# Performance work log

Measured on AMD Instinct MI355X. Metric: run time of the kernel, lower is better.

The kernel has to match this reference:

```python
import jax, jax.numpy as jnp
import numpy as np

N_WAY = 5
K_SHOT = 5
SEQ = 196          # patch tokens per image (ViT-S/16 @ 224)
TEMP = 0.0510310363  # similarity temperature ~ 1/sqrt(384)
LR = 0.1
OPT_STEPS = 15


def _normalize(emb):
    # [B, S, D] -> [B*S, D], rows L2-normalized with 1e-8 floor (matches torch.max(norm, 1e-8))
    v = emb.reshape(-1, emb.shape[-1])
    n = jnp.linalg.norm(v, axis=1, keepdims=True)
    return v / jnp.maximum(n, 1e-8)


def _block_mask():
    # block_diag of (SEQ x SEQ) blocks of -100 for each of the n_way*k_shot support images
    return jnp.kron(jnp.eye(N_WAY * K_SHOT, dtype=jnp.float32),
                    jnp.ones((SEQ, SEQ), jnp.float32)) * (-100.0)


def _predict(sup, qry, v, mask):
    # sup: [n_way*k_shot, S, D], qry: [Qb, Qs, D], v: [n_way*k_shot*S]
    S = sup.shape[1]
    Qb, Qs = qry.shape[0], qry.shape[1]
    C = _normalize(sup) @ _normalize(qry).T           # [Ls, Qb*Qs] cosine sims
    if mask is not None:
        C = C + mask
    pred = C + v[:, None]
    pred = pred.reshape(N_WAY, K_SHOT * S, Qb, Qs)
    pred = pred.transpose(0, 1, 3, 2).reshape(N_WAY, K_SHOT * S * Qs, Qb)
    pred = pred / TEMP
    pred = jax.scipy.special.logsumexp(pred, axis=1)  # [n_way, Qb]
    return pred.T                                     # [Qb, n_way]


def _optimize_v(sup_key, sup_query, labels, mask):
    # online SGD on the patch-embedding importance vector v (starts at zero)
    Ls = N_WAY * K_SHOT * sup_key.shape[1]
    B = sup_query.shape[0]

    def loss(v):
        p = _predict(sup_key, sup_query, v, mask)  # [B, n_way]
        logp = jax.nn.log_softmax(p, axis=1)
        return -jnp.mean(logp[jnp.arange(B), labels])

    def step(v, _):
        return v - LR * jax.grad(loss)(v), None

    v, _ = jax.lax.scan(step, jnp.zeros((Ls,), jnp.float32), None, length=OPT_STEPS)
    return v


def setup_inputs() -> dict:
    key = jax.random.key(0)
    k1, k2, k3, k4 = jax.random.split(key, 4)
    return {
        "support_emb_key": jax.random.normal(k1, (N_WAY * K_SHOT, SEQ, 384), jnp.float32),
        "support_emb_query": jax.random.normal(k2, (N_WAY * K_SHOT, SEQ, 384), jnp.float32),
        "query_emb": jax.random.normal(k3, (75, SEQ, 384), jnp.float32),
        "support_labels": jax.random.randint(k4, (N_WAY * K_SHOT,), 0, N_WAY, dtype=jnp.int32),
    }


def reference(support_emb_key, support_emb_query, query_emb, support_labels):
    mask = _block_mask()
    v = _optimize_v(support_emb_key, support_emb_query, support_labels, mask)
    return _predict(support_emb_key, query_emb, v, None)  # [75, n_way]
```

## Files before the change

kernel.cpp:

```cpp
#include <hip/hip_runtime.h>
#include <hip/hip_bf16.h>

#define NW 5
#define KS 5
#define SEQ 196
#define DIM 384
#define NSUP 25
#define NQRY 75
#define NIMG 100
#define LSUP 4900
#define LSUP_PAD 4992
#define QROWS 208
#define BLOCK_W 980
#define OPT_STEPS 15
#define MTILES 39
#define NSUPWG (NSUP * MTILES)
#define NQWG   (NQRY * MTILES)

static constexpr float TEMP_F = 0.0510310363f;
static constexpr float INV_T  = 1.0f / TEMP_F;
static constexpr float LR_F   = 0.1f;

typedef short v8s __attribute__((ext_vector_type(8)));
typedef float v4f __attribute__((ext_vector_type(4)));

__device__ inline unsigned short f2bf(float x) {
    unsigned int u = __float_as_uint(x);
    u += 0x7fffu + ((u >> 16) & 1u);
    return (unsigned short)(u >> 16);
}

__device__ __forceinline__ float fresh_f32(float* p) {
    return __hip_atomic_fetch_add(p, 0.0f, __ATOMIC_RELAXED, __HIP_MEMORY_SCOPE_AGENT);
}
__device__ __forceinline__ int fresh_i32(int* p) {
    return __hip_atomic_fetch_add(p, 0, __ATOMIC_RELAXED, __HIP_MEMORY_SCOPE_AGENT);
}
__device__ __forceinline__ unsigned fresh_u32(unsigned* p) {
    return __hip_atomic_fetch_add(p, 0u, __ATOMIC_RELAXED, __HIP_MEMORY_SCOPE_AGENT);
}

__global__ __launch_bounds__(256) void norm_all(const float* __restrict__ supk,
                                                const float* __restrict__ supq,
                                                const float* __restrict__ qry,
                                                unsigned short* __restrict__ Kb,
                                                unsigned short* __restrict__ Qall) {
    int R = blockIdx.x * 4 + (threadIdx.x >> 6);
    int l = threadIdx.x & 63;
    unsigned short* out;
    const float* in;
    float scale;
    if (R < LSUP_PAD) {
        out = Kb + (size_t)R * DIM;
        if (R >= LSUP) {
            #pragma unroll
            for (int k = 0; k < 6; ++k) out[l + 64 * k] = 0;
            return;
        }
        in = supk + (size_t)R * DIM;
        scale = INV_T;
    } else {
        int i = R - LSUP_PAD;
        int img = i / QROWS;
        int r = i - img * QROWS;
        out = Qall + (size_t)i * DIM;
        if (r >= SEQ) {
            #pragma unroll
            for (int k = 0; k < 6; ++k) out[l + 64 * k] = 0;
            return;
        }
        in = (img < NSUP)
            ? supq + ((size_t)img * SEQ + r) * DIM
            : qry  + ((size_t)(img - NSUP) * SEQ + r) * DIM;
        scale = 1.0f;
    }
    float x[6];
    #pragma unroll
    for (int k = 0; k < 6; ++k) x[k] = in[l + 64 * k];
    float s = 0.f;
    #pragma unroll
    for (int k = 0; k < 6; ++k) s += x[k] * x[k];
    #pragma unroll
    for (int m = 1; m < 64; m <<= 1) s += __shfl_xor(s, m);
    float sc = scale / fmaxf(sqrtf(s), 1e-8f);
    #pragma unroll
    for (int k = 0; k < 6; ++k) out[l + 64 * k] = f2bf(x[k] * sc);
}

#define MT  128
#define NTP 208
#define KCC 64

__device__ __forceinline__ void gload16(const void* g, void* l) {
    __builtin_amdgcn_global_load_lds(
        (__attribute__((address_space(1))) void*)g,
        (__attribute__((address_space(3))) void*)l, 16, 0, 0);
}

template<int IMG_BASE, int NWG, bool SUPPORT>
__device__ __forceinline__ void gemm_body(
    int gid,
    const unsigned short* __restrict__ Kb,
    const unsigned short* __restrict__ Qall,
    float* __restrict__ Rall,
    unsigned* done,
    unsigned short* Asm, unsigned short* Bsm)
{
    int t = threadIdx.x;

    constexpr int qq = NWG >> 3;
    constexpr int rr = NWG & 7;
    int xcd = gid & 7;
    int sub = gid >> 3;
    int L = (xcd < rr ? xcd * (qq + 1) : rr * (qq + 1) + (xcd - rr) * qq) + sub;
    int img = IMG_BASE + L / MTILES;
    int m_base = (L % MTILES) * MT;

    const unsigned short* Qimg = Qall + (size_t)img * (QROWS * DIM);

    int wv = t >> 6;
    int l  = t & 63;
    int lo = l & 15;
    int hi = l >> 4;
    int mh = (wv >> 1) * 64;
    int nh = wv & 1;

    int srow = l >> 3;
    int skp  = (l & 7) ^ srow;
    const unsigned short* aSrc = Kb   + (size_t)(m_base + wv * 32 + srow) * DIM + skp * 8;
    const unsigned short* bSrc = Qimg + (size_t)srow * DIM + skp * 8;

    v4f acc[4][7];
    #pragma unroll
    for (int m = 0; m < 4; ++m)
        #pragma unroll
        for (int n = 0; n < 7; ++n)
            acc[m][n] = (v4f){0.f, 0.f, 0.f, 0.f};

    for (int kb = 0; kb < DIM; kb += KCC) {
        #pragma unroll
        for (int j = 0; j < 4; ++j)
            gload16(aSrc + (size_t)j * 8 * DIM + kb,
                    Asm + (wv * 32 + j * 8) * KCC);
        #pragma unroll
        for (int jj = 0; jj < 7; ++jj) {
            int j = wv + jj * 4;
            if (j < 26)
                gload16(bSrc + (size_t)j * 8 * DIM + kb,
                        Bsm + j * 8 * KCC);
        }
        __syncthreads();

        const unsigned short* Ar = Asm + (mh + lo) * KCC;
        const unsigned short* Br = Bsm + (nh * 112 + lo) * KCC;
        #pragma unroll
        for (int kk = 0; kk < 2; ++kk) {
            int koff = ((hi + 4 * kk) ^ (lo & 7)) * 8;
            v8s a0 = *(const v8s*)(Ar + koff);
            v8s a1 = *(const v8s*)(Ar + 16 * KCC + koff);
            v8s a2 = *(const v8s*)(Ar + 32 * KCC + koff);
            v8s a3 = *(const v8s*)(Ar + 48 * KCC + koff);
            #pragma unroll
            for (int n = 0; n < 7; ++n) {
                if (nh == 0 || n < 6) {
                    v8s bb = *(const v8s*)(Br + n * 16 * KCC + koff);
                    acc[0][n] = __builtin_amdgcn_mfma_f32_16x16x32_bf16(a0, bb, acc[0][n], 0, 0, 0);
                    acc[1][n] = __builtin_amdgcn_mfma_f32_16x16x32_bf16(a1, bb, acc[1][n], 0, 0, 0);
                    acc[2][n] = __builtin_amdgcn_mfma_f32_16x16x32_bf16(a2, bb, acc[2][n], 0, 0, 0);
                    acc[3][n] = __builtin_amdgcn_mfma_f32_16x16x32_bf16(a3, bb, acc[3][n], 0, 0, 0);
                }
            }
        }
        __syncthreads();
    }

    float s[4][4];
    #pragma unroll
    for (int m = 0; m < 4; ++m)
        #pragma unroll
        for (int j = 0; j < 4; ++j) s[m][j] = 0.f;
    #pragma unroll
    for (int n = 0; n < 7; ++n) {
        if (nh == 0 || n < 6) {
            bool ok = ((nh * 7 + n) * 16 + lo) < SEQ;
            #pragma unroll
            for (int m = 0; m < 4; ++m)
                #pragma unroll
                for (int j = 0; j < 4; ++j)
                    s[m][j] += ok ? __expf(acc[m][n][j]) : 0.f;
        }
    }
    #pragma unroll
    for (int mm = 1; mm < 16; mm <<= 1) {
        #pragma unroll
        for (int m = 0; m < 4; ++m)
            #pragma unroll
            for (int j = 0; j < 4; ++j)
                s[m][j] += __shfl_xor(s[m][j], mm);
    }
    float* rp = (float*)Asm;
    if (lo == 0) {
        #pragma unroll
        for (int m = 0; m < 4; ++m)
            #pragma unroll
            for (int j = 0; j < 4; ++j)
                rp[nh * 128 + mh + m * 16 + hi * 4 + j] = s[m][j];
    }
    __syncthreads();
    if (t < MT) {
        int gr = m_base + t;
        if (gr < LSUP) {
            float o = rp[t] + rp[128 + t];
            if (img < NSUP && (gr / SEQ) == img) o = 0.f;
            if (SUPPORT)
                __hip_atomic_store(&Rall[(size_t)img * LSUP + gr], o,
                                   __ATOMIC_RELAXED, __HIP_MEMORY_SCOPE_AGENT);
            else
                Rall[(size_t)img * LSUP + gr] = o;
        }
    }
    if (SUPPORT) {
        __syncthreads();
        if (t == 0)
            __hip_atomic_fetch_add(done, 1u, __ATOMIC_RELAXED, __HIP_MEMORY_SCOPE_AGENT);
    }
}

__global__ __launch_bounds__(256, 3) void mega(
    const unsigned short* __restrict__ Kb,
    const unsigned short* __restrict__ Qall,
    float* __restrict__ Rall,
    const int* __restrict__ labels,
    float* __restrict__ Dbufs,
    int* __restrict__ flags,
    unsigned* __restrict__ done,
    float* __restrict__ e_out)
{
    __shared__ __align__(16) unsigned short Asm[MT * KCC];
    __shared__ __align__(16) unsigned short Bsm[NTP * KCC];

    if (blockIdx.x >= NW + NSUPWG) {
        gemm_body<NSUP, NQWG, false>((int)blockIdx.x - (NW + NSUPWG),
                                     Kb, Qall, Rall, done, Asm, Bsm);
        return;
    }
    if (blockIdx.x >= NW) {
        gemm_body<0, NSUPWG, true>((int)blockIdx.x - NW,
                                   Kb, Qall, Rall, done, Asm, Bsm);
        return;
    }

    float* sh  = (float*)Asm;
    float* red = sh;
    float* cfs = sh + 100;
    float* Dsm = sh + 128;
    int*   lsm = (int*)(sh + 256);

    int w = blockIdx.x;
    int t = threadIdx.x;
    int wave = t >> 6, lane = t & 63;

    if (t == 0) {
        while (fresh_u32(done) < (unsigned)NSUPWG)
            __builtin_amdgcn_s_sleep(8);
    }
    __syncthreads();

    float Rv[4][NSUP];
    #pragma unroll
    for (int b = 0; b < NSUP; ++b) {
        const float* Rb = Rall + (size_t)b * LSUP + w * BLOCK_W;
        Rv[0][b] = Rb[t];
        Rv[1][b] = Rb[t + 256];
        Rv[2][b] = Rb[t + 512];
        Rv[3][b] = (t < BLOCK_W - 768) ? Rb[t + 768] : 0.f;
    }
    if (t < NSUP) lsm[t] = labels[t];

    float e0 = 1.f, e1 = 1.f, e2 = 1.f, e3 = 1.f;
    float v0 = 0.f, v1 = 0.f, v2 = 0.f, v3 = 0.f;

    auto pushD = [&](int step) {
        float part[NSUP];
        #pragma unroll
        for (int b = 0; b < NSUP; ++b)
            part[b] = e0 * Rv[0][b] + e1 * Rv[1][b] + e2 * Rv[2][b] + e3 * Rv[3][b];
        #pragma unroll
        for (int b = 0; b < NSUP; ++b) {
            #pragma unroll
            for (int m = 32; m; m >>= 1) part[b] += __shfl_xor(part[b], m);
        }
        if (lane == 0) {
            #pragma unroll
            for (int b = 0; b < NSUP; ++b) red[wave * NSUP + b] = part[b];
        }
        __syncthreads();
        if (t < NSUP) {
            float s = red[t] + red[NSUP + t] + red[2 * NSUP + t] + red[3 * NSUP + t];
            __hip_atomic_store(&Dbufs[step * 125 + t * 5 + w], s,
                               __ATOMIC_RELAXED, __HIP_MEMORY_SCOPE_AGENT);
        }
        __syncthreads();
        if (t == 0)
            __hip_atomic_store(&flags[w], step + 1,
                               __ATOMIC_RELAXED, __HIP_MEMORY_SCOPE_AGENT);
    };

    pushD(0);

    for (int s = 0; s < OPT_STEPS; ++s) {
        if (wave == 0) {
            for (;;) {
                int f = (lane < NW) ? fresh_i32(&flags[lane]) : 0x7fffffff;
                if (__all(f >= s + 1)) break;
                __builtin_amdgcn_s_sleep(4);
            }
        }
        __syncthreads();
        if (t < 125)
            Dsm[t] = fresh_f32(&Dbufs[s * 125 + t]);
        __syncthreads();
        if (t < NSUP) {
            float Dsum = 0.f, Dw = 1.f;
            #pragma unroll
            for (int ww = 0; ww < NW; ++ww) {
                float d = Dsm[t * 5 + ww];
                Dsum += d;
                if (ww == w) Dw = d;
            }
            cfs[t] = ((Dw / Dsum) - (w == lsm[t] ? 1.f : 0.f)) * (INV_T / 25.f) / Dw;
        }
        __syncthreads();
        float g0 = 0.f, g1 = 0.f, g2 = 0.f, g3 = 0.f;
        #pragma unroll
        for (int b = 0; b < NSUP; ++b) {
            float c = cfs[b];
            g0 += c * Rv[0][b];
            g1 += c * Rv[1][b];
            g2 += c * Rv[2][b];
            g3 += c * Rv[3][b];
        }
        v0 -= LR_F * e0 * g0; e0 = __expf(v0 * INV_T);
        v1 -= LR_F * e1 * g1; e1 = __expf(v1 * INV_T);
        v2 -= LR_F * e2 * g2; e2 = __expf(v2 * INV_T);
        v3 -= LR_F * e3 * g3; e3 = __expf(v3 * INV_T);
        __syncthreads();
        if (s + 1 < OPT_STEPS) pushD(s + 1);
    }

    float* eo = e_out + w * BLOCK_W;
    eo[t]       = e0;
    eo[t + 256] = e1;
    eo[t + 512] = e2;
    if (t < BLOCK_W - 768) eo[t + 768] = e3;
}

__global__ __launch_bounds__(256) void final_pred(const float* __restrict__ Rall,
                                                  const float* __restrict__ e_out,
                                                  float* __restrict__ out) {
    __shared__ float ws[4];
    int blk = blockIdx.x;
    int qb = blk / 5, w = blk % 5;
    const float* R  = Rall + (size_t)(NSUP + qb) * LSUP + w * BLOCK_W;
    const float* eb = e_out + w * BLOCK_W;
    int t = threadIdx.x;
    float p = 0.f;
    for (int i = t; i < BLOCK_W; i += 256) p += eb[i] * R[i];
    #pragma unroll
    for (int m = 32; m; m >>= 1) p += __shfl_xor(p, m);
    if ((t & 63) == 0) ws[t >> 6] = p;
    __syncthreads();
    if (t == 0) out[blk] = logf(ws[0] + ws[1] + ws[2] + ws[3]);
}

extern "C" void kernel_launch(void* const* d_in, const int* in_sizes, int n_in,
                              void* d_out, int out_size, void* d_ws, size_t ws_size,
                              hipStream_t stream) {
    const float* sup_key = (const float*)d_in[0];
    const float* sup_qry = (const float*)d_in[1];
    const float* qry     = (const float*)d_in[2];
    const int*   labels  = (const int*)d_in[3];
    float* out = (float*)d_out;

    char* ws = (char*)d_ws;
    size_t off = 0;
    auto take = [&](size_t bytes) {
        char* p = ws + off;
        off = (off + bytes + 255) & ~(size_t)255;
        return p;
    };
    unsigned short* Kb   = (unsigned short*)take((size_t)LSUP_PAD * DIM * 2);
    unsigned short* Qall = (unsigned short*)take((size_t)NIMG * QROWS * DIM * 2);
    float*          Rall = (float*)take((size_t)NIMG * LSUP * 4);
    float*          Dbuf = (float*)take(((size_t)(OPT_STEPS + 1) * 125 + 64) * 4);
    float*          eout = (float*)take((size_t)LSUP * 4);
    int*            flags = (int*)(Dbuf + (OPT_STEPS + 1) * 125);
    unsigned*       done  = (unsigned*)(flags + 8);

    hipMemsetAsync(Dbuf, 0, ((size_t)(OPT_STEPS + 1) * 125 + 64) * 4, stream);

    norm_all<<<(LSUP_PAD + NIMG * QROWS) / 4, 256, 0, stream>>>(
        sup_key, sup_qry, qry, Kb, Qall);

    mega<<<NW + NSUPWG + NQWG, 256, 0, stream>>>(
        Kb, Qall, Rall, labels, Dbuf, flags, done, eout);

    final_pred<<<NQRY * NW, 256, 0, stream>>>(Rall, eout, out);
}
```

Measured before the change: 219.6 us.

## Place optimizer blocks on one XCD and sync via workgroup-scope L2 atomics

Result: slower. 254.9 us (+16.0%).

```diff
diff --git a/kernel.cpp b/kernel.cpp
--- a/kernel.cpp
+++ b/kernel.cpp
@@ -39,6 +39,9 @@
 __device__ __forceinline__ unsigned fresh_u32(unsigned* p) {
     return __hip_atomic_fetch_add(p, 0u, __ATOMIC_RELAXED, __HIP_MEMORY_SCOPE_AGENT);
 }
+__device__ __forceinline__ int l2_rmw_i32(int* p, int add) {
+    return __hip_atomic_fetch_add(p, add, __ATOMIC_RELAXED, __HIP_MEMORY_SCOPE_WORKGROUP);
+}
 
 __global__ __launch_bounds__(256) void norm_all(const float* __restrict__ supk,
                                                 const float* __restrict__ supq,
@@ -231,22 +234,25 @@
     const unsigned short* __restrict__ Qall,
     float* __restrict__ Rall,
     const int* __restrict__ labels,
-    float* __restrict__ Dbufs,
-    int* __restrict__ flags,
+    float* __restrict__ DbufL2,
+    float* __restrict__ DbufA,
+    int* __restrict__ flagsL2,
+    int* __restrict__ flagsA,
     unsigned* __restrict__ done,
     float* __restrict__ e_out)
 {
     __shared__ __align__(16) unsigned short Asm[MT * KCC];
     __shared__ __align__(16) unsigned short Bsm[NTP * KCC];
-
-    if (blockIdx.x >= NW + NSUPWG) {
-        gemm_body<NSUP, NQWG, false>((int)blockIdx.x - (NW + NSUPWG),
-                                     Kb, Qall, Rall, done, Asm, Bsm);
-        return;
-    }
-    if (blockIdx.x >= NW) {
-        gemm_body<0, NSUPWG, true>((int)blockIdx.x - NW,
-                                   Kb, Qall, Rall, done, Asm, Bsm);
+    __shared__ int smode;
+
+    int id = blockIdx.x;
+    bool isOpt = (id < 40) && ((id & 7) == 0);
+    if (!isOpt) {
+        int gid = (id < 40) ? id - ((id + 7) >> 3) : id - 5;
+        if (gid < NSUPWG)
+            gemm_body<0, NSUPWG, true>(gid, Kb, Qall, Rall, done, Asm, Bsm);
+        else
+            gemm_body<NSUP, NQWG, false>(gid - NSUPWG, Kb, Qall, Rall, done, Asm, Bsm);
         return;
     }
 
@@ -256,9 +262,10 @@
     float* Dsm = sh + 128;
     int*   lsm = (int*)(sh + 256);
 
-    int w = blockIdx.x;
+    int w = id >> 3;
     int t = threadIdx.x;
     int wave = t >> 6, lane = t & 63;
+    if (t == 0) smode = 1;
 
     if (t == 0) {
         while (fresh_u32(done) < (unsigned)NSUPWG)
@@ -297,28 +304,44 @@
         __syncthreads();
         if (t < NSUP) {
             float s = red[t] + red[NSUP + t] + red[2 * NSUP + t] + red[3 * NSUP + t];
-            __hip_atomic_store(&Dbufs[step * 125 + t * 5 + w], s,
+            DbufL2[step * 125 + t * 5 + w] = s;
+            __hip_atomic_store(&DbufA[step * 125 + t * 5 + w], s,
                                __ATOMIC_RELAXED, __HIP_MEMORY_SCOPE_AGENT);
         }
         __syncthreads();
-        if (t == 0)
-            __hip_atomic_store(&flags[w], step + 1,
+        if (t == 0) {
+            l2_rmw_i32(&flagsL2[w], 1);
+            __hip_atomic_store(&flagsA[w], step + 1,
                                __ATOMIC_RELAXED, __HIP_MEMORY_SCOPE_AGENT);
+        }
     };
 
     pushD(0);
 
     for (int s = 0; s < OPT_STEPS; ++s) {
         if (wave == 0) {
+            bool fast = (smode == 1);
+            unsigned long long t0 = __builtin_amdgcn_s_memrealtime();
             for (;;) {
-                int f = (lane < NW) ? fresh_i32(&flags[lane]) : 0x7fffffff;
-                if (__all(f >= s + 1)) break;
-                __builtin_amdgcn_s_sleep(4);
+                int f;
+                if (fast) {
+                    f = (lane < NW) ? l2_rmw_i32(&flagsL2[lane], 0) : 0x7fffffff;
+                    if (__all(f >= s + 1)) break;
+                    if (__builtin_amdgcn_s_memrealtime() - t0 > 2500ull) {
+                        fast = false;
+                        if (lane == 0) smode = 0;
+                    }
+                } else {
+                    f = (lane < NW) ? fresh_i32(&flagsA[lane]) : 0x7fffffff;
+                    if (__all(f >= s + 1)) break;
+                }
+                __builtin_amdgcn_s_sleep(1);
             }
         }
         __syncthreads();
         if (t < 125)
-            Dsm[t] = fresh_f32(&Dbufs[s * 125 + t]);
+            Dsm[t] = (smode == 1) ? DbufL2[s * 125 + t]
+                                  : fresh_f32(&DbufA[s * 125 + t]);
         __syncthreads();
         if (t < NSUP) {
             float Dsum = 0.f, Dw = 1.f;
@@ -389,21 +412,24 @@
         off = (off + bytes + 255) & ~(size_t)255;
         return p;
     };
-    unsigned short* Kb   = (unsigned short*)take((size_t)LSUP_PAD * DIM * 2);
-    unsigned short* Qall = (unsigned short*)take((size_t)NIMG * QROWS * DIM * 2);
-    float*          Rall = (float*)take((size_t)NIMG * LSUP * 4);
-    float*          Dbuf = (float*)take(((size_t)(OPT_STEPS + 1) * 125 + 64) * 4);
-    float*          eout = (float*)take((size_t)LSUP * 4);
-    int*            flags = (int*)(Dbuf + (OPT_STEPS + 1) * 125);
-    unsigned*       done  = (unsigned*)(flags + 8);
-
-    hipMemsetAsync(Dbuf, 0, ((size_t)(OPT_STEPS + 1) * 125 + 64) * 4, stream);
+    unsigned short* Kb     = (unsigned short*)take((size_t)LSUP_PAD * DIM * 2);
+    unsigned short* Qall   = (unsigned short*)take((size_t)NIMG * QROWS * DIM * 2);
+    float*          Rall   = (float*)take((size_t)NIMG * LSUP * 4);
+    float*          DbufL2 = (float*)take((size_t)(OPT_STEPS + 1) * 125 * 4);
+    float*          DbufA  = (float*)take((size_t)(OPT_STEPS + 1) * 125 * 4);
+    float*          eout   = (float*)take((size_t)LSUP * 4);
+    int*            fl     = (int*)take(64 * 4);
+    int*            flagsL2 = fl;
+    int*            flagsA  = fl + 8;
+    unsigned*       done    = (unsigned*)(fl + 16);
+
+    hipMemsetAsync(fl, 0, 64 * 4, stream);
 
     norm_all<<<(LSUP_PAD + NIMG * QROWS) / 4, 256, 0, stream>>>(
         sup_key, sup_qry, qry, Kb, Qall);
 
     mega<<<NW + NSUPWG + NQWG, 256, 0, stream>>>(
-        Kb, Qall, Rall, labels, Dbuf, flags, done, eout);
+        Kb, Qall, Rall, labels, DbufL2, DbufA, flagsL2, flagsA, done, eout);
 
     final_pred<<<NQRY * NW, 256, 0, stream>>>(Rall, eout, out);
 }
```

## Fuse final prediction into mega kernel with query-done counter and padded flags

Applied to the files above, without the earlier changes.

Result: slower. 319.7 us (+45.6%).

```diff
diff --git a/kernel.cpp b/kernel.cpp
--- a/kernel.cpp
+++ b/kernel.cpp
@@ -16,6 +16,7 @@
 #define MTILES 39
 #define NSUPWG (NSUP * MTILES)
 #define NQWG   (NQRY * MTILES)
+#define SPIN_LIMIT (1u << 22)
 
 static constexpr float TEMP_F = 0.0510310363f;
 static constexpr float INV_T  = 1.0f / TEMP_F;
@@ -38,6 +39,12 @@
 }
 __device__ __forceinline__ unsigned fresh_u32(unsigned* p) {
     return __hip_atomic_fetch_add(p, 0u, __ATOMIC_RELAXED, __HIP_MEMORY_SCOPE_AGENT);
+}
+__device__ __forceinline__ void agent_store_f32(float* p, float v) {
+    __hip_atomic_store(p, v, __ATOMIC_RELAXED, __HIP_MEMORY_SCOPE_AGENT);
+}
+__device__ __forceinline__ void agent_store_i32(int* p, int v) {
+    __hip_atomic_store(p, v, __ATOMIC_RELAXED, __HIP_MEMORY_SCOPE_AGENT);
 }
 
 __global__ __launch_bounds__(256) void norm_all(const float* __restrict__ supk,
@@ -97,13 +104,13 @@
         (__attribute__((address_space(3))) void*)l, 16, 0, 0);
 }
 
-template<int IMG_BASE, int NWG, bool SUPPORT>
+template<int IMG_BASE, int NWG>
 __device__ __forceinline__ void gemm_body(
     int gid,
     const unsigned short* __restrict__ Kb,
     const unsigned short* __restrict__ Qall,
     float* __restrict__ Rall,
-    unsigned* done,
+    unsigned* counter,
     unsigned short* Asm, unsigned short* Bsm)
 {
     int t = threadIdx.x;
@@ -212,18 +219,12 @@
         if (gr < LSUP) {
             float o = rp[t] + rp[128 + t];
             if (img < NSUP && (gr / SEQ) == img) o = 0.f;
-            if (SUPPORT)
-                __hip_atomic_store(&Rall[(size_t)img * LSUP + gr], o,
-                                   __ATOMIC_RELAXED, __HIP_MEMORY_SCOPE_AGENT);
-            else
-                Rall[(size_t)img * LSUP + gr] = o;
-        }
-    }
-    if (SUPPORT) {
-        __syncthreads();
-        if (t == 0)
-            __hip_atomic_fetch_add(done, 1u, __ATOMIC_RELAXED, __HIP_MEMORY_SCOPE_AGENT);
-    }
+            agent_store_f32(&Rall[(size_t)img * LSUP + gr], o);
+        }
+    }
+    __syncthreads();
+    if (t == 0)
+        __hip_atomic_fetch_add(counter, 1u, __ATOMIC_RELAXED, __HIP_MEMORY_SCOPE_AGENT);
 }
 
 __global__ __launch_bounds__(256, 3) void mega(
@@ -231,22 +232,22 @@
     const unsigned short* __restrict__ Qall,
     float* __restrict__ Rall,
     const int* __restrict__ labels,
-    float* __restrict__ Dbufs,
+    float* __restrict__ Dbuf,
     int* __restrict__ flags,
-    unsigned* __restrict__ done,
-    float* __restrict__ e_out)
+    unsigned* __restrict__ sdone,
+    unsigned* __restrict__ qdone,
+    float* __restrict__ out)
 {
     __shared__ __align__(16) unsigned short Asm[MT * KCC];
     __shared__ __align__(16) unsigned short Bsm[NTP * KCC];
 
-    if (blockIdx.x >= NW + NSUPWG) {
-        gemm_body<NSUP, NQWG, false>((int)blockIdx.x - (NW + NSUPWG),
-                                     Kb, Qall, Rall, done, Asm, Bsm);
+    int id = blockIdx.x;
+    if (id >= NW + NSUPWG) {
+        gemm_body<NSUP, NQWG>(id - (NW + NSUPWG), Kb, Qall, Rall, qdone, Asm, Bsm);
         return;
     }
-    if (blockIdx.x >= NW) {
-        gemm_body<0, NSUPWG, true>((int)blockIdx.x - NW,
-                                   Kb, Qall, Rall, done, Asm, Bsm);
+    if (id >= NW) {
+        gemm_body<0, NSUPWG>(id - NW, Kb, Qall, Rall, sdone, Asm, Bsm);
         return;
     }
 
@@ -254,14 +255,17 @@
     float* red = sh;
     float* cfs = sh + 100;
     float* Dsm = sh + 128;
-    int*   lsm = (int*)(sh + 256);
-
-    int w = blockIdx.x;
+    float* myD = sh + 256;
+    int*   lsm = (int*)(sh + 288);
+    float* esm = (float*)Bsm;
+
+    int w = id;
     int t = threadIdx.x;
     int wave = t >> 6, lane = t & 63;
 
     if (t == 0) {
-        while (fresh_u32(done) < (unsigned)NSUPWG)
+        unsigned spins = 0;
+        while (fresh_u32(sdone) < (unsigned)NSUPWG && ++spins < SPIN_LIMIT)
             __builtin_amdgcn_s_sleep(8);
     }
     __syncthreads();
@@ -297,28 +301,33 @@
         __syncthreads();
         if (t < NSUP) {
             float s = red[t] + red[NSUP + t] + red[2 * NSUP + t] + red[3 * NSUP + t];
-            __hip_atomic_store(&Dbufs[step * 125 + t * 5 + w], s,
-                               __ATOMIC_RELAXED, __HIP_MEMORY_SCOPE_AGENT);
+            myD[t] = s;
+            agent_store_f32(&Dbuf[(step * NW + w) * 32 + t], s);
         }
         __syncthreads();
         if (t == 0)
-            __hip_atomic_store(&flags[w], step + 1,
-                               __ATOMIC_RELAXED, __HIP_MEMORY_SCOPE_AGENT);
+            agent_store_i32(&flags[w * 32], step + 1);
     };
 
     pushD(0);
 
     for (int s = 0; s < OPT_STEPS; ++s) {
         if (wave == 0) {
+            unsigned spins = 0;
             for (;;) {
-                int f = (lane < NW) ? fresh_i32(&flags[lane]) : 0x7fffffff;
+                int f = (lane < NW) ? fresh_i32(&flags[lane * 32]) : 0x7fffffff;
                 if (__all(f >= s + 1)) break;
-                __builtin_amdgcn_s_sleep(4);
+                if (++spins >= SPIN_LIMIT) break;
+                __builtin_amdgcn_s_sleep(1);
             }
         }
         __syncthreads();
-        if (t < 125)
-            Dsm[t] = fresh_f32(&Dbufs[s * 125 + t]);
+        if (t < 125) {
+            int wp = t / 25, b = t - wp * 25;
+            float dv = (wp == w) ? myD[b]
+                                 : fresh_f32(&Dbuf[(s * NW + wp) * 32 + b]);
+            Dsm[b * 5 + wp] = dv;
+        }
         __syncthreads();
         if (t < NSUP) {
             float Dsum = 0.f, Dw = 1.f;
@@ -348,29 +357,24 @@
         if (s + 1 < OPT_STEPS) pushD(s + 1);
     }
 
-    float* eo = e_out + w * BLOCK_W;
-    eo[t]       = e0;
-    eo[t + 256] = e1;
-    eo[t + 512] = e2;
-    if (t < BLOCK_W - 768) eo[t + 768] = e3;
-}
-
-__global__ __launch_bounds__(256) void final_pred(const float* __restrict__ Rall,
-                                                  const float* __restrict__ e_out,
-                                                  float* __restrict__ out) {
-    __shared__ float ws[4];
-    int blk = blockIdx.x;
-    int qb = blk / 5, w = blk % 5;
-    const float* R  = Rall + (size_t)(NSUP + qb) * LSUP + w * BLOCK_W;
-    const float* eb = e_out + w * BLOCK_W;
-    int t = threadIdx.x;
-    float p = 0.f;
-    for (int i = t; i < BLOCK_W; i += 256) p += eb[i] * R[i];
-    #pragma unroll
-    for (int m = 32; m; m >>= 1) p += __shfl_xor(p, m);
-    if ((t & 63) == 0) ws[t >> 6] = p;
+    esm[t] = e0;
+    esm[t + 256] = e1;
+    esm[t + 512] = e2;
+    if (t < BLOCK_W - 768) esm[t + 768] = e3;
+    if (t == 0) {
+        unsigned spins = 0;
+        while (fresh_u32(qdone) < (unsigned)NQWG && ++spins < SPIN_LIMIT)
+            __builtin_amdgcn_s_sleep(8);
+    }
     __syncthreads();
-    if (t == 0) out[blk] = logf(ws[0] + ws[1] + ws[2] + ws[3]);
+    for (int qb = wave; qb < NQRY; qb += 4) {
+        const float* R = Rall + (size_t)(NSUP + qb) * LSUP + w * BLOCK_W;
+        float p = 0.f;
+        for (int i = lane; i < BLOCK_W; i += 64) p += esm[i] * R[i];
+        #pragma unroll
+        for (int m = 32; m; m >>= 1) p += __shfl_xor(p, m);
+        if (lane == 0) out[qb * 5 + w] = logf(p);
+    }
 }
 
 extern "C" void kernel_launch(void* const* d_in, const int* in_sizes, int n_in,
@@ -392,18 +396,18 @@
     unsigned short* Kb   = (unsigned short*)take((size_t)LSUP_PAD * DIM * 2);
     unsigned short* Qall = (unsigned short*)take((size_t)NIMG * QROWS * DIM * 2);
     float*          Rall = (float*)take((size_t)NIMG * LSUP * 4);
-    float*          Dbuf = (float*)take(((size_t)(OPT_STEPS + 1) * 125 + 64) * 4);
-    float*          eout = (float*)take((size_t)LSUP * 4);
-    int*            flags = (int*)(Dbuf + (OPT_STEPS + 1) * 125);
-    unsigned*       done  = (unsigned*)(flags + 8);
-
-    hipMemsetAsync(Dbuf, 0, ((size_t)(OPT_STEPS + 1) * 125 + 64) * 4, stream);
+    float*          Dbuf = (float*)take((size_t)16 * NW * 32 * 4);
+    int*            fl   = (int*)take(256 * 4);
+    int*            flags = fl;
+    unsigned*       sdone = (unsigned*)(fl + 192);
+    unsigned*       qdone = (unsigned*)(fl + 224);
+
+    hipMemsetAsync(Dbuf, 0, (size_t)16 * NW * 32 * 4, stream);
+    hipMemsetAsync(fl, 0, 256 * 4, stream);
 
     norm_all<<<(LSUP_PAD + NIMG * QROWS) / 4, 256, 0, stream>>>(
         sup_key, sup_qry, qry, Kb, Qall);
 
     mega<<<NW + NSUPWG + NQWG, 256, 0, stream>>>(
-        Kb, Qall, Rall, labels, Dbuf, flags, done, eout);
-
-    final_pred<<<NQRY * NW, 256, 0, stream>>>(Rall, eout, out);
-}
+        Kb, Qall, Rall, labels, Dbuf, flags, sdone, qdone, out);
+}
```
